# Kernel tuning notes

Measured on AMD Instinct MI355X. Metric: run time of the kernel, lower is better.

The kernel has to match this reference:

```python
import jax, jax.numpy as jnp
import numpy as np

B, S, H, E, K, DFF = 4, 2048, 1024, 8, 2, 4096


def setup_inputs() -> dict:
    key = jax.random.key(0)
    k0, k1, k2, k3 = jax.random.split(key, 4)
    sc = 0.02
    return {
        "x": jax.random.normal(k0, (B, S, H), jnp.float32),
        "gate_W": jax.random.normal(k1, (H, E), jnp.float32) * sc,
        "gate_b": jnp.zeros((E,), jnp.float32),
        "W1": jax.random.normal(k2, (H, DFF), jnp.float32) * sc,
        "b1": jnp.zeros((DFF,), jnp.float32),
        "W2": jax.random.normal(k3, (DFF, H), jnp.float32) * sc,
        "b2": jnp.zeros((H,), jnp.float32),
    }


def reference(x, gate_W, gate_b, W1, b1, W2, b2):
    b, s, h = x.shape
    x_flat = x.reshape(-1, h)                      # [T, H]
    gate_scores = x_flat @ gate_W + gate_b         # [T, E]
    top_k_scores, top_k_idx = jax.lax.top_k(gate_scores, K)   # [T, K]
    top_k_w = jax.nn.softmax(top_k_scores, axis=-1)           # [T, K]

    # All experts share the same weights (ModuleList reuses one module), so
    # sum_i w_i * expert_i(x) == expert(x) * sum_i w_i. top_k indices are
    # unique per token, so the per-token combine weight is sum of top-k weights.
    hdd = jax.nn.gelu(x_flat @ W1 + b1, approximate=False)    # [T, DFF]
    y = hdd @ W2 + b2                                         # [T, H]
    tok_w = top_k_w.sum(axis=-1)                              # [T] (== 1.0)
    output = (y * tok_w[:, None]).reshape(b, s, h)

    expert_load = gate_scores.mean(axis=0)                    # [E]
    aux_loss = (expert_load ** 2).sum()
    exp_counts = jnp.zeros((E,), jnp.int32).at[top_k_idx.ravel()].add(1)
    return output, aux_loss, exp_counts
```

## Files before the change

kernel.cpp:

```cpp
#include <hip/hip_runtime.h>
#include <hip/hip_bf16.h>
#include <math.h>

#define Tn   8192
#define Hn   1024
#define En   8
#define DFFn 4096

typedef __attribute__((ext_vector_type(8))) short bf16x8;
typedef __attribute__((ext_vector_type(8))) unsigned short u16x8;
typedef __attribute__((ext_vector_type(4))) float f32x4;

static __device__ inline unsigned short f2bf(float f) {
    __hip_bfloat16 h = __float2bfloat16(f);
    return __builtin_bit_cast(unsigned short, h);
}

__global__ __launch_bounds__(256) void prep(
    const float* __restrict__ W1, unsigned short* __restrict__ W1t,
    const float* __restrict__ W2, unsigned short* __restrict__ W2t,
    const float* __restrict__ x, const float* __restrict__ gW,
    const float* __restrict__ gb, unsigned short* __restrict__ xbf,
    float* __restrict__ tokw, float* __restrict__ pb_load,
    int* __restrict__ pb_cnt)
{
    __shared__ float smem[8 * 1024 + En];
    __shared__ int   s_cnt[En];
    const int tid = threadIdx.x;
    const int id  = blockIdx.x;

    if (id < 512) {
        const float* src; unsigned short* dst; int SR, SC, tb;
        if (id < 256) { src = W1; dst = W1t; SR = Hn;   SC = DFFn; tb = id; }
        else          { src = W2; dst = W2t; SR = DFFn; SC = Hn;   tb = id - 256; }
        const int tcs = SC >> 7;
        const int tr  = tb / tcs, tc = tb - tr * tcs;
        const int r0  = tr << 7, c0 = tc << 7;
        unsigned short* tile = (unsigned short*)smem;

        #pragma unroll
        for (int i = 0; i < 16; ++i) {
            int idx = tid + i * 256;
            int r = idx >> 5, c4 = (idx & 31) << 2;
            float4 v = *(const float4*)(src + (size_t)(r0 + r) * SC + c0 + c4);
            int cs = c4 ^ (((r >> 3) & 7) << 2);
            ushort4 pk;
            pk.x = f2bf(v.x); pk.y = f2bf(v.y);
            pk.z = f2bf(v.z); pk.w = f2bf(v.w);
            *(ushort4*)(tile + r * 128 + cs) = pk;
        }
        __syncthreads();
        #pragma unroll
        for (int i = 0; i < 8; ++i) {
            int idx = tid + i * 256;
            int n = idx >> 4, kg = idx & 15, k0 = kg << 3;
            int s = (kg & 7) << 2;
            u16x8 o;
            #pragma unroll
            for (int j = 0; j < 8; ++j)
                o[j] = tile[(k0 + j) * 128 + (n ^ s)];
            *(u16x8*)(dst + (size_t)(c0 + n) * SR + r0 + k0) = o;
        }
        return;
    }

    const int gid = id - 512;
    float* gwt    = smem;
    float* s_load = smem + 8 * 1024;
    if (tid < En) { s_load[tid] = 0.f; s_cnt[tid] = 0; }
    #pragma unroll
    for (int i = 0; i < 8; ++i) {
        int f4 = tid + i * 256;
        float4 v = ((const float4*)gW)[f4];
        int f = f4 << 2;
        gwt[((f + 0) & 7) * 1024 + ((f + 0) >> 3)] = v.x;
        gwt[((f + 1) & 7) * 1024 + ((f + 1) >> 3)] = v.y;
        gwt[((f + 2) & 7) * 1024 + ((f + 2) >> 3)] = v.z;
        gwt[((f + 3) & 7) * 1024 + ((f + 3) >> 3)] = v.w;
    }
    __syncthreads();

    const int lane = tid & 63;
    const int wv   = tid >> 6;

    for (int tok = gid * 4 + wv; tok < Tn; tok += 1024) {
        const float4* xr = (const float4*)(x + (size_t)tok * Hn);
        float acc[8] = {0.f,0.f,0.f,0.f,0.f,0.f,0.f,0.f};
        #pragma unroll
        for (int j = 0; j < Hn / 256; ++j) {
            int h4 = j * 64 + lane;
            float4 xv = xr[h4];
            ushort4 pk;
            pk.x = f2bf(xv.x); pk.y = f2bf(xv.y);
            pk.z = f2bf(xv.z); pk.w = f2bf(xv.w);
            ((ushort4*)xbf)[(size_t)tok * (Hn / 4) + h4] = pk;
            #pragma unroll
            for (int e = 0; e < 8; ++e) {
                const float4 w = *(const float4*)(gwt + e * 1024 + h4 * 4);
                acc[e] += xv.x * w.x + xv.y * w.y + xv.z * w.z + xv.w * w.w;
            }
        }
        #pragma unroll
        for (int e = 0; e < 8; ++e) {
            float v = acc[e];
            #pragma unroll
            for (int off = 32; off > 0; off >>= 1) v += __shfl_xor(v, off, 64);
            acc[e] = v + gb[e];
        }
        if (lane == 0) {
            #pragma unroll
            for (int e = 0; e < 8; ++e) atomicAdd(&s_load[e], acc[e]);
            int i1 = 0; float v1 = acc[0];
            #pragma unroll
            for (int e = 1; e < 8; ++e) if (acc[e] > v1) { v1 = acc[e]; i1 = e; }
            int i2 = -1; float v2 = -3.0e38f;
            #pragma unroll
            for (int e = 0; e < 8; ++e) if (e != i1 && acc[e] > v2) { v2 = acc[e]; i2 = e; }
            atomicAdd(&s_cnt[i1], 1);
            atomicAdd(&s_cnt[i2], 1);
            float e2 = __expf(v2 - v1);
            float t  = 1.0f + e2;
            tokw[tok] = 1.0f / t + e2 / t;
        }
    }
    __syncthreads();
    if (tid < En) {
        pb_load[gid * En + tid] = s_load[tid];
        pb_cnt [gid * En + tid] = s_cnt[tid];
    }
}

static __device__ inline bf16x8 ldsfrag(const char* base, int row, int chunk) {
    return *(const bf16x8*)(base + row * 128 + (((chunk) ^ (row & 7)) << 4));
}

template<int BN, int WM, int WN, int EPI>
__global__ __launch_bounds__(512, 2) void gemm8(
    const __hip_bfloat16* __restrict__ A,
    const __hip_bfloat16* __restrict__ Bt,
    const float* __restrict__ bias,
    const float* __restrict__ tokw,
    void* __restrict__ C, int N, int K, int nx,
    const float* __restrict__ pb_load, const int* __restrict__ pb_cnt,
    float* __restrict__ out_tail, int nblk)
{
    constexpr int BM = 256;
    constexpr int MR = (BM / WM) / 16;
    constexpr int NR = (BN / WN) / 16;
    constexpr int AU = BM / 64;
    constexpr int BU = BN / 64;
    constexpr int ABYTES = BM * 64 * 2;
    constexpr int BBYTES = BN * 64 * 2;
    constexpr int TILEB  = ABYTES + BBYTES;

    extern __shared__ char lds[];

    const int tid = threadIdx.x;
    const int id  = blockIdx.x;

    if (EPI == 0 && id >= nblk) {
        float* sl = (float*)lds;
        int*   sc = (int*)(lds + 64);
        if (tid < En) { sl[tid] = 0.f; sc[tid] = 0; }
        __syncthreads();
        const int e = tid & 7;
        float p = 0.f; int c = 0;
        for (int g = tid >> 3; g < 256; g += 64) {
            p += pb_load[g * En + e];
            c += pb_cnt [g * En + e];
        }
        atomicAdd(&sl[e], p);
        atomicAdd(&sc[e], c);
        __syncthreads();
        if (tid == 0) {
            float aux = 0.f;
            #pragma unroll
            for (int e2 = 0; e2 < En; ++e2) {
                float m = sl[e2] * (1.0f / (float)Tn);
                aux += m * m;
            }
            out_tail[0] = aux;
            #pragma unroll
            for (int e2 = 0; e2 < En; ++e2) out_tail[1 + e2] = (float)sc[e2];
        }
        return;
    }

    int wg = id;
    { int xcd = wg & 7, idx = wg >> 3; wg = xcd * (nblk >> 3) + idx; }
    const int by = wg / nx, bx = wg % nx;
    const int m0 = by * BM, n0 = bx * BN;

    const int lane = tid & 63;
    const int wid  = tid >> 6;
    const int wn   = wid % WN;
    const int wm   = wid / WN;
    const int wrow = wm * (BM / WM);
    const int wcol = wn * (BN / WN);
    const int fr   = lane & 15;
    const int fq   = lane >> 4;

    const int sr = tid >> 3;
    const int sc = (tid & 7) ^ (sr & 7);
    unsigned aOff[AU], bOff[BU];
    #pragma unroll
    for (int u = 0; u < AU; ++u)
        aOff[u] = (unsigned)((m0 + u * 64 + sr) * K + sc * 8);
    #pragma unroll
    for (int u = 0; u < BU; ++u)
        bOff[u] = (unsigned)((n0 + u * 64 + sr) * K + sc * 8);

#define STA(b, u, kt) __builtin_amdgcn_global_load_lds( \
    (const __attribute__((address_space(1))) void*)(A + aOff[u] + (unsigned)(kt) * 64u), \
    (__attribute__((address_space(3))) void*)(lds + (b) * TILEB + (u) * 8192 + tid * 16), 16, 0, 0)
#define STB(b, u, kt) __builtin_amdgcn_global_load_lds( \
    (const __attribute__((address_space(1))) void*)(Bt + bOff[u] + (unsigned)(kt) * 64u), \
    (__attribute__((address_space(3))) void*)(lds + (b) * TILEB + ABYTES + (u) * 8192 + tid * 16), 16, 0, 0)

    bf16x8 af[MR / 2][2];
    bf16x8 bfr[4][2];
    f32x4  acc[MR][NR];
    const f32x4 zero = {0.f, 0.f, 0.f, 0.f};
    #pragma unroll
    for (int i = 0; i < MR; ++i)
        #pragma unroll
        for (int j = 0; j < NR; ++j) acc[i][j] = zero;

#define RDA(b, half) do { _Pragma("unroll") \
    for (int m_ = 0; m_ < MR / 2; ++m_) { _Pragma("unroll") \
        for (int ks_ = 0; ks_ < 2; ++ks_) \
            af[m_][ks_] = ldsfrag(lds + (b) * TILEB, \
                wrow + ((half) * (MR / 2) + m_) * 16 + fr, ks_ * 4 + fq); } } while (0)

#define RDB(b, half) do { _Pragma("unroll") \
    for (int n_ = 0; n_ < 2; ++n_) { _Pragma("unroll") \
        for (int ks_ = 0; ks_ < 2; ++ks_) \
            bfr[(half) * 2 + n_][ks_] = ldsfrag(lds + (b) * TILEB + ABYTES, \
                wcol + ((half) * 2 + n_) * 16 + fr, ks_ * 4 + fq); } } while (0)

#define MFMAQ(hm, hn) do { \
    __builtin_amdgcn_s_setprio(1); \
    _Pragma("unroll") \
    for (int m_ = 0; m_ < MR / 2; ++m_) { _Pragma("unroll") \
        for (int n_ = 0; n_ < 2; ++n_) { _Pragma("unroll") \
            for (int ks_ = 0; ks_ < 2; ++ks_) \
                acc[(hm) * (MR / 2) + m_][(hn) * 2 + n_] = \
                    __builtin_amdgcn_mfma_f32_16x16x32_bf16( \
                        af[m_][ks_], bfr[(hn) * 2 + n_][ks_], \
                        acc[(hm) * (MR / 2) + m_][(hn) * 2 + n_], 0, 0, 0); } } \
    __builtin_amdgcn_s_setprio(0); } while (0)

#define MFMA1_N(hm, nn) do { _Pragma("unroll") \
    for (int m_ = 0; m_ < MR / 2; ++m_) { _Pragma("unroll") \
        for (int ks_ = 0; ks_ < 2; ++ks_) \
            acc[(hm) * (MR / 2) + m_][nn] = \
                __builtin_amdgcn_mfma_f32_16x16x32_bf16( \
                    bfr[nn][ks_], af[m_][ks_], \
                    acc[(hm) * (MR / 2) + m_][nn], 0, 0, 0); } } while (0)
#define MFMA1_M(hm, m_) do { _Pragma("unroll") \
    for (int n_ = 0; n_ < NR; ++n_) { _Pragma("unroll") \
        for (int ks_ = 0; ks_ < 2; ++ks_) \
            acc[(hm) * (MR / 2) + (m_)][n_] = \
                __builtin_amdgcn_mfma_f32_16x16x32_bf16( \
                    bfr[n_][ks_], af[m_][ks_], \
                    acc[(hm) * (MR / 2) + (m_)][n_], 0, 0, 0); } } while (0)

#define RD_A1(b, half, m_) do { _Pragma("unroll") \
    for (int ks_ = 0; ks_ < 2; ++ks_) \
        af[m_][ks_] = ldsfrag(lds + (b) * TILEB, \
            wrow + ((half) * (MR / 2) + (m_)) * 16 + fr, ks_ * 4 + fq); } while (0)
#define RD_B1(b, nn) do { _Pragma("unroll") \
    for (int ks_ = 0; ks_ < 2; ++ks_) \
        bfr[nn][ks_] = ldsfrag(lds + (b) * TILEB + ABYTES, \
            wcol + (nn) * 16 + fr, ks_ * 4 + fq); } while (0)

#define MIDSYNC do { \
    __builtin_amdgcn_sched_barrier(0); \
    __builtin_amdgcn_s_barrier(); \
    asm volatile("s_waitcnt lgkmcnt(0)" ::: "memory"); \
    __builtin_amdgcn_sched_barrier(0); } while (0)

#define SBARR do { \
    __builtin_amdgcn_sched_barrier(0); \
    __builtin_amdgcn_s_barrier(); \
    __builtin_amdgcn_sched_barrier(0); } while (0)

#define WAITL(n) do { \
    asm volatile("s_waitcnt lgkmcnt(" #n ")" ::: "memory"); \
    __builtin_amdgcn_sched_barrier(0); } while (0)

#define DRAIN6 do { asm volatile("s_waitcnt vmcnt(6)" ::: "memory"); \
    __builtin_amdgcn_sched_barrier(0); } while (0)
#define DRAIN2 do { asm volatile("s_waitcnt vmcnt(2)" ::: "memory"); \
    __builtin_amdgcn_sched_barrier(0); } while (0)
#define PRIO1 __builtin_amdgcn_s_setprio(1)
#define PRIO0 __builtin_amdgcn_s_setprio(0)

    const int KT = K >> 6;

    if constexpr (WM == 2) {
        STA(0,0,0); STA(0,1,0); STA(0,2,0); STA(0,3,0);
        STB(0,0,0); STB(0,1,0); STB(0,2,0); STB(0,3,0);
        STA(1,0,1); STA(1,2,1);
        STB(1,0,1); STB(1,1,1); STB(1,2,1); STB(1,3,1);
        DRAIN6;
        __builtin_amdgcn_s_barrier();
        __builtin_amdgcn_sched_barrier(0);

        for (int i = 0; i < (KT >> 1); ++i) {
            const int t1 = 2 * i + 1;
            const int c2 = (2 * i + 2 < KT) ? 2 * i + 2 : KT - 1;
            const int c3 = (2 * i + 3 < KT) ? 2 * i + 3 : KT - 1;

            RDA(0, 0); RDB(0, 0);
            STA(1,1,t1); STA(1,3,t1);
            MIDSYNC; MFMAQ(0, 0); SBARR;
            RDB(0, 1);
            STA(0,0,c2); STA(0,2,c2);
            MIDSYNC; MFMAQ(0, 1); SBARR;
            RDA(0, 1);
            STB(0,0,c2); STB(0,1,c2);
            MIDSYNC; MFMAQ(1, 0); SBARR;
            STB(0,2,c2); STB(0,3,c2);
            MIDSYNC; MFMAQ(1, 1); DRAIN6; SBARR;
            RDA(1, 0); RDB(1, 0);
            STA(0,1,c2); STA(0,3,c2);
            MIDSYNC; MFMAQ(0, 0); SBARR;
            RDB(1, 1);
            STA(1,0,c3); STA(1,2,c3);
            MIDSYNC; MFMAQ(0, 1); SBARR;
            RDA(1, 1);
            STB(1,0,c3); STB(1,1,c3);
            MIDSYNC; MFMAQ(1, 0); SBARR;
            STB(1,2,c3); STB(1,3,c3);
            MIDSYNC; MFMAQ(1, 1); DRAIN6; SBARR;
        }

        float bias4[NR];
        #pragma unroll
        for (int ni = 0; ni < NR; ++ni)
            bias4[ni] = bias[n0 + wcol + ni * 16 + fr];
        #pragma unroll
        for (int mi = 0; mi < MR; ++mi) {
            #pragma unroll
            for (int ni = 0; ni < NR; ++ni) {
                const int col = n0 + wcol + ni * 16 + fr;
                const int rb  = m0 + wrow + mi * 16 + fq * 4;
                #pragma unroll
                for (int i2 = 0; i2 < 4; ++i2) {
                    float u  = acc[mi][ni][i2] + bias4[ni];
                    float uu = u * u;
                    float z  = u * __fmaf_rn(uu, -0.07135607f, -1.59576912f);
                    float e  = __expf(z);
                    float g  = u * __builtin_amdgcn_rcpf(1.0f + e);
                    ((__hip_bfloat16*)C)[(size_t)(rb + i2) * N + col] =
                        __float2bfloat16(g);
                }
            }
        }
    } else {
        STA(0,0,0); STA(0,1,0); STA(0,2,0); STA(0,3,0);
        STB(0,0,0); STB(0,1,0);
        STB(1,0,1); STB(1,1,1);
        DRAIN2;
        __builtin_amdgcn_s_barrier();
        __builtin_amdgcn_sched_barrier(0);

        for (int i = 0; i < (KT >> 1); ++i) {
            const int t1 = 2 * i + 1;
            const int c2 = (2 * i + 2 < KT) ? 2 * i + 2 : KT - 1;
            const int c3 = (2 * i + 3 < KT) ? 2 * i + 3 : KT - 1;

            RD_A1(0,0,0); RD_A1(0,0,1);
            RD_B1(0,0); RD_B1(0,1); RD_B1(0,2); RD_B1(0,3);
            STA(1,0,t1); STA(1,1,t1); STA(1,2,t1); STA(1,3,t1);
            SBARR; PRIO1;
            WAITL(6); MFMA1_N(0,0);
            WAITL(4); MFMA1_N(0,1);
            WAITL(2); MFMA1_N(0,2);
            WAITL(0); MFMA1_N(0,3);
            PRIO0; SBARR;
            RD_A1(0,1,0); RD_A1(0,1,1);
            STB(0,0,c2); STB(0,1,c2);
            SBARR; PRIO1;
            WAITL(2); MFMA1_M(1,0);
            WAITL(0); MFMA1_M(1,1);
            PRIO0; DRAIN2; SBARR;
            RD_A1(1,0,0); RD_A1(1,0,1);
            RD_B1(1,0); RD_B1(1,1); RD_B1(1,2); RD_B1(1,3);
            STA(0,0,c2); STA(0,1,c2); STA(0,2,c2); STA(0,3,c2);
            SBARR; PRIO1;
            WAITL(6); MFMA1_N(0,0);
            WAITL(4); MFMA1_N(0,1);
            WAITL(2); MFMA1_N(0,2);
            WAITL(0); MFMA1_N(0,3);
            PRIO0; SBARR;
            RD_A1(1,1,0); RD_A1(1,1,1);
            STB(1,0,c3); STB(1,1,c3);
            SBARR; PRIO1;
            WAITL(2); MFMA1_M(1,0);
            WAITL(0); MFMA1_M(1,1);
            PRIO0; DRAIN2; SBARR;
        }

        const int mrow0 = m0 + wrow + fr;
        const int ncol0 = n0 + wcol + fq * 4;
        float4 b4[NR];
        #pragma unroll
        for (int ni = 0; ni < NR; ++ni)
            b4[ni] = *(const float4*)(bias + ncol0 + ni * 16);

        #pragma unroll
        for (int mi = 0; mi < MR; ++mi) {
            const int row = mrow0 + mi * 16;
            const float tw = tokw[row];
            #pragma unroll
            for (int ni = 0; ni < NR; ++ni) {
                f32x4 v = acc[mi][ni];
                float4 o;
                o.x = (v[0] + b4[ni].x) * tw;
                o.y = (v[1] + b4[ni].y) * tw;
                o.z = (v[2] + b4[ni].z) * tw;
                o.w = (v[3] + b4[ni].w) * tw;
                *(float4*)((float*)C + (size_t)row * N + ncol0 + ni * 16) = o;
            }
        }
    }

#undef STA
#undef STB
#undef RDA
#undef RDB
#undef RD_A1
#undef RD_B1
#undef MFMAQ
#undef MFMA1_N
#undef MFMA1_M
#undef MIDSYNC
#undef SBARR
#undef WAITL
#undef DRAIN6
#undef DRAIN2
#undef PRIO1
#undef PRIO0
}

extern "C" void kernel_launch(void* const* d_in, const int* in_sizes, int n_in,
                              void* d_out, int out_size, void* d_ws, size_t ws_size,
                              hipStream_t stream)
{
    const float* x  = (const float*)d_in[0];
    const float* gW = (const float*)d_in[1];
    const float* gb = (const float*)d_in[2];
    const float* W1 = (const float*)d_in[3];
    const float* b1 = (const float*)d_in[4];
    const float* W2 = (const float*)d_in[5];
    const float* b2 = (const float*)d_in[6];
    float* out = (float*)d_out;

    char* ws = (char*)d_ws;
    __hip_bfloat16* xbf = (__hip_bfloat16*)ws;  ws += (size_t)Tn * Hn * 2;
    __hip_bfloat16* W1t = (__hip_bfloat16*)ws;  ws += (size_t)Hn * DFFn * 2;
    __hip_bfloat16* W2t = (__hip_bfloat16*)ws;  ws += (size_t)Hn * DFFn * 2;
    __hip_bfloat16* hdd = (__hip_bfloat16*)ws;  ws += (size_t)Tn * DFFn * 2;
    float* tokw     = (float*)ws;               ws += (size_t)Tn * 4;
    float* pb_load  = (float*)ws;               ws += 256 * En * 4;
    int*   pb_cnt   = (int*)ws;                 ws += 256 * En * 4;

    static bool attr_done = false;
    if (!attr_done) {
        (void)hipFuncSetAttribute(
            reinterpret_cast<const void*>(&gemm8<256, 2, 4, 0>),
            hipFuncAttributeMaxDynamicSharedMemorySize, 131072);
        (void)hipFuncSetAttribute(
            reinterpret_cast<const void*>(&gemm8<128, 4, 2, 1>),
            hipFuncAttributeMaxDynamicSharedMemorySize, 98304);
        attr_done = true;
    }

    prep<<<768, 256, 0, stream>>>(W1, (unsigned short*)W1t,
                                  W2, (unsigned short*)W2t,
                                  x, gW, gb, (unsigned short*)xbf,
                                  tokw, pb_load, pb_cnt);

    gemm8<256, 2, 4, 0><<<513, 512, 131072, stream>>>(
        xbf, W1t, b1, nullptr, hdd, DFFn, Hn, 16,
        pb_load, pb_cnt, out + (size_t)Tn * Hn, 512);

    gemm8<128, 4, 2, 1><<<256, 512, 98304, stream>>>(
        hdd, W2t, b2, tokw, out, Hn, DFFn, 8,
        nullptr, nullptr, nullptr, 256);
}
```

Measured before the change: 262.9 us.

## Fuse prep and both GEMMs into one cooperative persistent kernel with grid syncs

```diff
diff --git a/kernel.cpp b/kernel.cpp
--- a/kernel.cpp
+++ b/kernel.cpp
@@ -1,6 +1,9 @@
 #include <hip/hip_runtime.h>
 #include <hip/hip_bf16.h>
+#include <hip/hip_cooperative_groups.h>
 #include <math.h>
+
+namespace cg = cooperative_groups;
 
 #define Tn   8192
 #define Hn   1024
@@ -16,161 +19,147 @@
     return __builtin_bit_cast(unsigned short, h);
 }
 
-__global__ __launch_bounds__(256) void prep(
-    const float* __restrict__ W1, unsigned short* __restrict__ W1t,
-    const float* __restrict__ W2, unsigned short* __restrict__ W2t,
-    const float* __restrict__ x, const float* __restrict__ gW,
-    const float* __restrict__ gb, unsigned short* __restrict__ xbf,
-    float* __restrict__ tokw, float* __restrict__ pb_load,
-    int* __restrict__ pb_cnt)
-{
-    __shared__ float smem[8 * 1024 + En];
-    __shared__ int   s_cnt[En];
-    const int tid = threadIdx.x;
-    const int id  = blockIdx.x;
-
-    if (id < 512) {
-        const float* src; unsigned short* dst; int SR, SC, tb;
-        if (id < 256) { src = W1; dst = W1t; SR = Hn;   SC = DFFn; tb = id; }
-        else          { src = W2; dst = W2t; SR = DFFn; SC = Hn;   tb = id - 256; }
-        const int tcs = SC >> 7;
-        const int tr  = tb / tcs, tc = tb - tr * tcs;
-        const int r0  = tr << 7, c0 = tc << 7;
-        unsigned short* tile = (unsigned short*)smem;
-
-        #pragma unroll
-        for (int i = 0; i < 16; ++i) {
-            int idx = tid + i * 256;
-            int r = idx >> 5, c4 = (idx & 31) << 2;
-            float4 v = *(const float4*)(src + (size_t)(r0 + r) * SC + c0 + c4);
-            int cs = c4 ^ (((r >> 3) & 7) << 2);
-            ushort4 pk;
-            pk.x = f2bf(v.x); pk.y = f2bf(v.y);
-            pk.z = f2bf(v.z); pk.w = f2bf(v.w);
-            *(ushort4*)(tile + r * 128 + cs) = pk;
-        }
-        __syncthreads();
-        #pragma unroll
-        for (int i = 0; i < 8; ++i) {
-            int idx = tid + i * 256;
-            int n = idx >> 4, kg = idx & 15, k0 = kg << 3;
-            int s = (kg & 7) << 2;
-            u16x8 o;
-            #pragma unroll
-            for (int j = 0; j < 8; ++j)
-                o[j] = tile[(k0 + j) * 128 + (n ^ s)];
-            *(u16x8*)(dst + (size_t)(c0 + n) * SR + r0 + k0) = o;
-        }
-        return;
-    }
-
-    const int gid = id - 512;
-    float* gwt    = smem;
-    float* s_load = smem + 8 * 1024;
-    if (tid < En) { s_load[tid] = 0.f; s_cnt[tid] = 0; }
-    #pragma unroll
-    for (int i = 0; i < 8; ++i) {
-        int f4 = tid + i * 256;
-        float4 v = ((const float4*)gW)[f4];
-        int f = f4 << 2;
-        gwt[((f + 0) & 7) * 1024 + ((f + 0) >> 3)] = v.x;
-        gwt[((f + 1) & 7) * 1024 + ((f + 1) >> 3)] = v.y;
-        gwt[((f + 2) & 7) * 1024 + ((f + 2) >> 3)] = v.z;
-        gwt[((f + 3) & 7) * 1024 + ((f + 3) >> 3)] = v.w;
-    }
-    __syncthreads();
-
-    const int lane = tid & 63;
-    const int wv   = tid >> 6;
-
-    for (int tok = gid * 4 + wv; tok < Tn; tok += 1024) {
-        const float4* xr = (const float4*)(x + (size_t)tok * Hn);
-        float acc[8] = {0.f,0.f,0.f,0.f,0.f,0.f,0.f,0.f};
-        #pragma unroll
-        for (int j = 0; j < Hn / 256; ++j) {
-            int h4 = j * 64 + lane;
-            float4 xv = xr[h4];
-            ushort4 pk;
-            pk.x = f2bf(xv.x); pk.y = f2bf(xv.y);
-            pk.z = f2bf(xv.z); pk.w = f2bf(xv.w);
-            ((ushort4*)xbf)[(size_t)tok * (Hn / 4) + h4] = pk;
-            #pragma unroll
-            for (int e = 0; e < 8; ++e) {
-                const float4 w = *(const float4*)(gwt + e * 1024 + h4 * 4);
-                acc[e] += xv.x * w.x + xv.y * w.y + xv.z * w.z + xv.w * w.w;
-            }
-        }
-        #pragma unroll
-        for (int e = 0; e < 8; ++e) {
-            float v = acc[e];
-            #pragma unroll
-            for (int off = 32; off > 0; off >>= 1) v += __shfl_xor(v, off, 64);
-            acc[e] = v + gb[e];
-        }
-        if (lane == 0) {
-            #pragma unroll
-            for (int e = 0; e < 8; ++e) atomicAdd(&s_load[e], acc[e]);
-            int i1 = 0; float v1 = acc[0];
-            #pragma unroll
-            for (int e = 1; e < 8; ++e) if (acc[e] > v1) { v1 = acc[e]; i1 = e; }
-            int i2 = -1; float v2 = -3.0e38f;
-            #pragma unroll
-            for (int e = 0; e < 8; ++e) if (e != i1 && acc[e] > v2) { v2 = acc[e]; i2 = e; }
-            atomicAdd(&s_cnt[i1], 1);
-            atomicAdd(&s_cnt[i2], 1);
-            float e2 = __expf(v2 - v1);
-            float t  = 1.0f + e2;
-            tokw[tok] = 1.0f / t + e2 / t;
-        }
-    }
-    __syncthreads();
-    if (tid < En) {
-        pb_load[gid * En + tid] = s_load[tid];
-        pb_cnt [gid * En + tid] = s_cnt[tid];
-    }
-}
-
 static __device__ inline bf16x8 ldsfrag(const char* base, int row, int chunk) {
     return *(const bf16x8*)(base + row * 128 + (((chunk) ^ (row & 7)) << 4));
 }
 
-template<int BN, int WM, int WN, int EPI>
-__global__ __launch_bounds__(512, 2) void gemm8(
-    const __hip_bfloat16* __restrict__ A,
-    const __hip_bfloat16* __restrict__ Bt,
-    const float* __restrict__ bias,
-    const float* __restrict__ tokw,
-    void* __restrict__ C, int N, int K, int nx,
-    const float* __restrict__ pb_load, const int* __restrict__ pb_cnt,
-    float* __restrict__ out_tail, int nblk)
+__global__ __launch_bounds__(512, 2) void moe_fused(
+    const float* __restrict__ x,  const float* __restrict__ gW,
+    const float* __restrict__ gb, const float* __restrict__ W1,
+    const float* __restrict__ b1, const float* __restrict__ W2,
+    const float* __restrict__ b2,
+    unsigned short* __restrict__ W1t, unsigned short* __restrict__ W2t,
+    unsigned short* __restrict__ xbf, unsigned short* __restrict__ hdd,
+    float* __restrict__ tokw, float* __restrict__ pb_load,
+    int* __restrict__ pb_cnt, float* __restrict__ out,
+    float* __restrict__ out_tail)
 {
-    constexpr int BM = 256;
-    constexpr int MR = (BM / WM) / 16;
-    constexpr int NR = (BN / WN) / 16;
-    constexpr int AU = BM / 64;
-    constexpr int BU = BN / 64;
-    constexpr int ABYTES = BM * 64 * 2;
-    constexpr int BBYTES = BN * 64 * 2;
-    constexpr int TILEB  = ABYTES + BBYTES;
-
     extern __shared__ char lds[];
-
     const int tid = threadIdx.x;
-    const int id  = blockIdx.x;
-
-    if (EPI == 0 && id >= nblk) {
+    const int bid = blockIdx.x;
+    const int lane = tid & 63;
+    const int wid  = tid >> 6;
+    const int fr   = lane & 15;
+    const int fq   = lane >> 4;
+    const int sr   = tid >> 3;
+    const int scq  = (tid & 7) ^ (sr & 7);
+
+    {
+        unsigned short* tile = (unsigned short*)lds;
+        #pragma unroll
+        for (int pass = 0; pass < 2; ++pass) {
+            const float* src = pass ? W2 : W1;
+            unsigned short* dst = pass ? W2t : W1t;
+            const int SR = pass ? DFFn : Hn, SC = pass ? Hn : DFFn;
+            const int tcs = SC >> 7;
+            const int tr = bid / tcs, tc = bid - tr * tcs;
+            const int r0 = tr << 7, c0 = tc << 7;
+            #pragma unroll
+            for (int i = 0; i < 8; ++i) {
+                int idx = tid + i * 512;
+                int r = idx >> 5, c4 = (idx & 31) << 2;
+                float4 v = *(const float4*)(src + (size_t)(r0 + r) * SC + c0 + c4);
+                int cs = c4 ^ (((r >> 3) & 7) << 2);
+                ushort4 pk;
+                pk.x = f2bf(v.x); pk.y = f2bf(v.y);
+                pk.z = f2bf(v.z); pk.w = f2bf(v.w);
+                *(ushort4*)(tile + r * 128 + cs) = pk;
+            }
+            __syncthreads();
+            #pragma unroll
+            for (int i = 0; i < 4; ++i) {
+                int idx = tid + i * 512;
+                int n = idx >> 4, kg = idx & 15, k0 = kg << 3;
+                int s = (kg & 7) << 2;
+                u16x8 o;
+                #pragma unroll
+                for (int j = 0; j < 8; ++j)
+                    o[j] = tile[(k0 + j) * 128 + (n ^ s)];
+                *(u16x8*)(dst + (size_t)(c0 + n) * SR + r0 + k0) = o;
+            }
+            __syncthreads();
+        }
+
+        float* gwt    = (float*)lds;
+        float* s_load = (float*)(lds + 32768);
+        int*   s_cnt  = (int*)(lds + 32768 + 64);
+        if (tid < En) { s_load[tid] = 0.f; s_cnt[tid] = 0; }
+        #pragma unroll
+        for (int i = 0; i < 4; ++i) {
+            int f4 = tid + i * 512;
+            float4 v = ((const float4*)gW)[f4];
+            int f = f4 << 2;
+            gwt[((f + 0) & 7) * 1024 + ((f + 0) >> 3)] = v.x;
+            gwt[((f + 1) & 7) * 1024 + ((f + 1) >> 3)] = v.y;
+            gwt[((f + 2) & 7) * 1024 + ((f + 2) >> 3)] = v.z;
+            gwt[((f + 3) & 7) * 1024 + ((f + 3) >> 3)] = v.w;
+        }
+        __syncthreads();
+        #pragma unroll
+        for (int t = 0; t < 4; ++t) {
+            const int tok = bid * 32 + wid + t * 8;
+            const float4* xr = (const float4*)(x + (size_t)tok * Hn);
+            float acc[8] = {0.f,0.f,0.f,0.f,0.f,0.f,0.f,0.f};
+            #pragma unroll
+            for (int j = 0; j < Hn / 256; ++j) {
+                int h4 = j * 64 + lane;
+                float4 xv = xr[h4];
+                ushort4 pk;
+                pk.x = f2bf(xv.x); pk.y = f2bf(xv.y);
+                pk.z = f2bf(xv.z); pk.w = f2bf(xv.w);
+                ((ushort4*)xbf)[(size_t)tok * (Hn / 4) + h4] = pk;
+                #pragma unroll
+                for (int e = 0; e < 8; ++e) {
+                    const float4 w = *(const float4*)(gwt + e * 1024 + h4 * 4);
+                    acc[e] += xv.x * w.x + xv.y * w.y + xv.z * w.z + xv.w * w.w;
+                }
+            }
+            #pragma unroll
+            for (int e = 0; e < 8; ++e) {
+                float v = acc[e];
+                #pragma unroll
+                for (int off = 32; off > 0; off >>= 1) v += __shfl_xor(v, off, 64);
+                acc[e] = v + gb[e];
+            }
+            if (lane == 0) {
+                #pragma unroll
+                for (int e = 0; e < 8; ++e) atomicAdd(&s_load[e], acc[e]);
+                int i1 = 0; float v1 = acc[0];
+                #pragma unroll
+                for (int e = 1; e < 8; ++e) if (acc[e] > v1) { v1 = acc[e]; i1 = e; }
+                int i2 = -1; float v2 = -3.0e38f;
+                #pragma unroll
+                for (int e = 0; e < 8; ++e) if (e != i1 && acc[e] > v2) { v2 = acc[e]; i2 = e; }
+                atomicAdd(&s_cnt[i1], 1);
+                atomicAdd(&s_cnt[i2], 1);
+                float e2 = __expf(v2 - v1);
+                float tt = 1.0f + e2;
+                tokw[tok] = 1.0f / tt + e2 / tt;
+            }
+        }
+        __syncthreads();
+        if (tid < En) {
+            pb_load[bid * En + tid] = s_load[tid];
+            pb_cnt [bid * En + tid] = s_cnt[tid];
+        }
+    }
+
+    __threadfence();
+    cg::this_grid().sync();
+
+    if (bid == 0) {
         float* sl = (float*)lds;
-        int*   sc = (int*)(lds + 64);
-        if (tid < En) { sl[tid] = 0.f; sc[tid] = 0; }
+        int*   scp = (int*)(lds + 64);
+        if (tid < En) { sl[tid] = 0.f; scp[tid] = 0; }
         __syncthreads();
         const int e = tid & 7;
         float p = 0.f; int c = 0;
-        for (int g = tid >> 3; g < 256; g += 64) {
-            p += pb_load[g * En + e];
-            c += pb_cnt [g * En + e];
+        for (int g2 = tid >> 3; g2 < 256; g2 += 64) {
+            p += pb_load[g2 * En + e];
+            c += pb_cnt [g2 * En + e];
         }
         atomicAdd(&sl[e], p);
-        atomicAdd(&sc[e], c);
+        atomicAdd(&scp[e], c);
         __syncthreads();
         if (tid == 0) {
             float aux = 0.f;
@@ -181,266 +170,305 @@
             }
             out_tail[0] = aux;
             #pragma unroll
-            for (int e2 = 0; e2 < En; ++e2) out_tail[1 + e2] = (float)sc[e2];
-        }
-        return;
+            for (int e2 = 0; e2 < En; ++e2) out_tail[1 + e2] = (float)scp[e2];
+        }
+        __syncthreads();
     }
 
-    int wg = id;
-    { int xcd = wg & 7, idx = wg >> 3; wg = xcd * (nblk >> 3) + idx; }
-    const int by = wg / nx, bx = wg % nx;
-    const int m0 = by * BM, n0 = bx * BN;
-
-    const int lane = tid & 63;
-    const int wid  = tid >> 6;
-    const int wn   = wid % WN;
-    const int wm   = wid / WN;
-    const int wrow = wm * (BM / WM);
-    const int wcol = wn * (BN / WN);
-    const int fr   = lane & 15;
-    const int fq   = lane >> 4;
-
-    const int sr = tid >> 3;
-    const int sc = (tid & 7) ^ (sr & 7);
-    unsigned aOff[AU], bOff[BU];
-    #pragma unroll
-    for (int u = 0; u < AU; ++u)
-        aOff[u] = (unsigned)((m0 + u * 64 + sr) * K + sc * 8);
-    #pragma unroll
-    for (int u = 0; u < BU; ++u)
-        bOff[u] = (unsigned)((n0 + u * 64 + sr) * K + sc * 8);
-
-#define STA(b, u, kt) __builtin_amdgcn_global_load_lds( \
-    (const __attribute__((address_space(1))) void*)(A + aOff[u] + (unsigned)(kt) * 64u), \
-    (__attribute__((address_space(3))) void*)(lds + (b) * TILEB + (u) * 8192 + tid * 16), 16, 0, 0)
-#define STB(b, u, kt) __builtin_amdgcn_global_load_lds( \
-    (const __attribute__((address_space(1))) void*)(Bt + bOff[u] + (unsigned)(kt) * 64u), \
-    (__attribute__((address_space(3))) void*)(lds + (b) * TILEB + ABYTES + (u) * 8192 + tid * 16), 16, 0, 0)
-
-    bf16x8 af[MR / 2][2];
-    bf16x8 bfr[4][2];
-    f32x4  acc[MR][NR];
-    const f32x4 zero = {0.f, 0.f, 0.f, 0.f};
-    #pragma unroll
-    for (int i = 0; i < MR; ++i)
-        #pragma unroll
-        for (int j = 0; j < NR; ++j) acc[i][j] = zero;
-
-#define RDA(b, half) do { _Pragma("unroll") \
-    for (int m_ = 0; m_ < MR / 2; ++m_) { _Pragma("unroll") \
-        for (int ks_ = 0; ks_ < 2; ++ks_) \
-            af[m_][ks_] = ldsfrag(lds + (b) * TILEB, \
-                wrow + ((half) * (MR / 2) + m_) * 16 + fr, ks_ * 4 + fq); } } while (0)
-
-#define RDB(b, half) do { _Pragma("unroll") \
-    for (int n_ = 0; n_ < 2; ++n_) { _Pragma("unroll") \
-        for (int ks_ = 0; ks_ < 2; ++ks_) \
-            bfr[(half) * 2 + n_][ks_] = ldsfrag(lds + (b) * TILEB + ABYTES, \
-                wcol + ((half) * 2 + n_) * 16 + fr, ks_ * 4 + fq); } } while (0)
-
-#define MFMAQ(hm, hn) do { \
-    __builtin_amdgcn_s_setprio(1); \
-    _Pragma("unroll") \
-    for (int m_ = 0; m_ < MR / 2; ++m_) { _Pragma("unroll") \
-        for (int n_ = 0; n_ < 2; ++n_) { _Pragma("unroll") \
-            for (int ks_ = 0; ks_ < 2; ++ks_) \
-                acc[(hm) * (MR / 2) + m_][(hn) * 2 + n_] = \
-                    __builtin_amdgcn_mfma_f32_16x16x32_bf16( \
-                        af[m_][ks_], bfr[(hn) * 2 + n_][ks_], \
-                        acc[(hm) * (MR / 2) + m_][(hn) * 2 + n_], 0, 0, 0); } } \
-    __builtin_amdgcn_s_setprio(0); } while (0)
-
-#define MFMA1_N(hm, nn) do { _Pragma("unroll") \
-    for (int m_ = 0; m_ < MR / 2; ++m_) { _Pragma("unroll") \
-        for (int ks_ = 0; ks_ < 2; ++ks_) \
-            acc[(hm) * (MR / 2) + m_][nn] = \
-                __builtin_amdgcn_mfma_f32_16x16x32_bf16( \
-                    bfr[nn][ks_], af[m_][ks_], \
-                    acc[(hm) * (MR / 2) + m_][nn], 0, 0, 0); } } while (0)
-#define MFMA1_M(hm, m_) do { _Pragma("unroll") \
-    for (int n_ = 0; n_ < NR; ++n_) { _Pragma("unroll") \
-        for (int ks_ = 0; ks_ < 2; ++ks_) \
-            acc[(hm) * (MR / 2) + (m_)][n_] = \
-                __builtin_amdgcn_mfma_f32_16x16x32_bf16( \
-                    bfr[n_][ks_], af[m_][ks_], \
-                    acc[(hm) * (MR / 2) + (m_)][n_], 0, 0, 0); } } while (0)
-
-#define RD_A1(b, half, m_) do { _Pragma("unroll") \
-    for (int ks_ = 0; ks_ < 2; ++ks_) \
-        af[m_][ks_] = ldsfrag(lds + (b) * TILEB, \
-            wrow + ((half) * (MR / 2) + (m_)) * 16 + fr, ks_ * 4 + fq); } while (0)
-#define RD_B1(b, nn) do { _Pragma("unroll") \
-    for (int ks_ = 0; ks_ < 2; ++ks_) \
-        bfr[nn][ks_] = ldsfrag(lds + (b) * TILEB + ABYTES, \
-            wcol + (nn) * 16 + fr, ks_ * 4 + fq); } while (0)
-
+#define SBARR do { \
+    __builtin_amdgcn_sched_barrier(0); \
+    __builtin_amdgcn_s_barrier(); \
+    __builtin_amdgcn_sched_barrier(0); } while (0)
 #define MIDSYNC do { \
     __builtin_amdgcn_sched_barrier(0); \
     __builtin_amdgcn_s_barrier(); \
     asm volatile("s_waitcnt lgkmcnt(0)" ::: "memory"); \
     __builtin_amdgcn_sched_barrier(0); } while (0)
-
-#define SBARR do { \
-    __builtin_amdgcn_sched_barrier(0); \
-    __builtin_amdgcn_s_barrier(); \
-    __builtin_amdgcn_sched_barrier(0); } while (0)
-
 #define WAITL(n) do { \
     asm volatile("s_waitcnt lgkmcnt(" #n ")" ::: "memory"); \
     __builtin_amdgcn_sched_barrier(0); } while (0)
-
-#define DRAIN6 do { asm volatile("s_waitcnt vmcnt(6)" ::: "memory"); \
-    __builtin_amdgcn_sched_barrier(0); } while (0)
-#define DRAIN2 do { asm volatile("s_waitcnt vmcnt(2)" ::: "memory"); \
+#define VMC(n) do { asm volatile("s_waitcnt vmcnt(" #n ")" ::: "memory"); \
     __builtin_amdgcn_sched_barrier(0); } while (0)
 #define PRIO1 __builtin_amdgcn_s_setprio(1)
 #define PRIO0 __builtin_amdgcn_s_setprio(0)
 
-    const int KT = K >> 6;
-
-    if constexpr (WM == 2) {
-        STA(0,0,0); STA(0,1,0); STA(0,2,0); STA(0,3,0);
-        STB(0,0,0); STB(0,1,0); STB(0,2,0); STB(0,3,0);
-        STA(1,0,1); STA(1,2,1);
-        STB(1,0,1); STB(1,1,1); STB(1,2,1); STB(1,3,1);
-        DRAIN6;
+    {
+        constexpr int ABY = 256 * 64 * 2;
+        constexpr int TLB = ABY + ABY;
+        const int wn = wid & 3, wm = wid >> 2;
+        const int wrow = wm * 128, wcol = wn * 64;
+
+        bf16x8 af[4][2], bfr[4][2];
+        f32x4  acc[8][4];
+        const f32x4 zero = {0.f, 0.f, 0.f, 0.f};
+
+#define STA0(b, u, kt) __builtin_amdgcn_global_load_lds( \
+    (const __attribute__((address_space(1))) void*)(xbf + aOff[u] + (unsigned)(kt) * 64u), \
+    (__attribute__((address_space(3))) void*)(lds + (b) * TLB + (u) * 8192 + tid * 16), 16, 0, 0)
+#define STB0(b, u, kt) __builtin_amdgcn_global_load_lds( \
+    (const __attribute__((address_space(1))) void*)(W1t + bOff[u] + (unsigned)(kt) * 64u), \
+    (__attribute__((address_space(3))) void*)(lds + (b) * TLB + ABY + (u) * 8192 + tid * 16), 16, 0, 0)
+#define RDA0(b, half) do { _Pragma("unroll") \
+    for (int m_ = 0; m_ < 4; ++m_) { _Pragma("unroll") \
+        for (int ks_ = 0; ks_ < 2; ++ks_) \
+            af[m_][ks_] = ldsfrag(lds + (b) * TLB, \
+                wrow + ((half) * 4 + m_) * 16 + fr, ks_ * 4 + fq); } } while (0)
+#define RDB0(b, half) do { _Pragma("unroll") \
+    for (int n_ = 0; n_ < 2; ++n_) { _Pragma("unroll") \
+        for (int ks_ = 0; ks_ < 2; ++ks_) \
+            bfr[(half) * 2 + n_][ks_] = ldsfrag(lds + (b) * TLB + ABY, \
+                wcol + ((half) * 2 + n_) * 16 + fr, ks_ * 4 + fq); } } while (0)
+#define MFMAQ0(hm, hn) do { \
+    PRIO1; \
+    _Pragma("unroll") \
+    for (int m_ = 0; m_ < 4; ++m_) { _Pragma("unroll") \
+        for (int n_ = 0; n_ < 2; ++n_) { _Pragma("unroll") \
+            for (int ks_ = 0; ks_ < 2; ++ks_) \
+                acc[(hm) * 4 + m_][(hn) * 2 + n_] = \
+                    __builtin_amdgcn_mfma_f32_16x16x32_bf16( \
+                        af[m_][ks_], bfr[(hn) * 2 + n_][ks_], \
+                        acc[(hm) * 4 + m_][(hn) * 2 + n_], 0, 0, 0); } } \
+    PRIO0; } while (0)
+
+        for (int tt = 0; tt < 2; ++tt) {
+            const int g   = bid + tt * 256;
+            const int xcd = g & 7;
+            const int wg  = xcd * 64 + (g >> 3);
+            const int by  = wg >> 4, bx = wg & 15;
+            const int m0  = by * 256, n0 = bx * 256;
+
+            unsigned aOff[4], bOff[4];
+            #pragma unroll
+            for (int u = 0; u < 4; ++u) {
+                aOff[u] = (unsigned)((m0 + u * 64 + sr) * Hn + scq * 8);
+                bOff[u] = (unsigned)((n0 + u * 64 + sr) * Hn + scq * 8);
+            }
+            #pragma unroll
+            for (int i = 0; i < 8; ++i)
+                #pragma unroll
+                for (int j = 0; j < 4; ++j) acc[i][j] = zero;
+
+            STA0(0,0,0); STA0(0,1,0); STA0(0,2,0); STA0(0,3,0);
+            STB0(0,0,0); STB0(0,1,0); STB0(0,2,0); STB0(0,3,0);
+            STA0(1,0,1); STA0(1,2,1);
+            STB0(1,0,1); STB0(1,1,1); STB0(1,2,1); STB0(1,3,1);
+            VMC(6);
+            __builtin_amdgcn_s_barrier();
+            __builtin_amdgcn_sched_barrier(0);
+
+            const int KT = Hn >> 6;
+            for (int i = 0; i < (KT >> 1); ++i) {
+                const int t1 = 2 * i + 1;
+                const int c2 = (2 * i + 2 < KT) ? 2 * i + 2 : KT - 1;
+                const int c3 = (2 * i + 3 < KT) ? 2 * i + 3 : KT - 1;
+
+                RDA0(0, 0); RDB0(0, 0);
+                STA0(1,1,t1); STA0(1,3,t1);
+                MIDSYNC; MFMAQ0(0, 0); SBARR;
+
+                RDB0(0, 1);
+                STA0(0,0,c2); STA0(0,2,c2);
+                MIDSYNC; MFMAQ0(0, 1); SBARR;
+
+                RDA0(0, 1);
+                STB0(0,0,c2); STB0(0,1,c2);
+                MIDSYNC; MFMAQ0(1, 0); SBARR;
+
+                STB0(0,2,c2); STB0(0,3,c2);
+                MIDSYNC; MFMAQ0(1, 1); VMC(6); SBARR;
+
+                RDA0(1, 0); RDB0(1, 0);
+                STA0(0,1,c2); STA0(0,3,c2);
+                MIDSYNC; MFMAQ0(0, 0); SBARR;
+
+                RDB0(1, 1);
+                STA0(1,0,c3); STA0(1,2,c3);
+                MIDSYNC; MFMAQ0(0, 1); SBARR;
+
+                RDA0(1, 1);
+                STB0(1,0,c3); STB0(1,1,c3);
+                MIDSYNC; MFMAQ0(1, 0); SBARR;
+
+                STB0(1,2,c3); STB0(1,3,c3);
+                MIDSYNC; MFMAQ0(1, 1); VMC(6); SBARR;
+            }
+
+            float bias4[4];
+            #pragma unroll
+            for (int ni = 0; ni < 4; ++ni)
+                bias4[ni] = b1[n0 + wcol + ni * 16 + fr];
+            #pragma unroll
+            for (int mi = 0; mi < 8; ++mi) {
+                #pragma unroll
+                for (int ni = 0; ni < 4; ++ni) {
+                    const int col = n0 + wcol + ni * 16 + fr;
+                    const int rb  = m0 + wrow + mi * 16 + fq * 4;
+                    #pragma unroll
+                    for (int i2 = 0; i2 < 4; ++i2) {
+                        float u  = acc[mi][ni][i2] + bias4[ni];
+                        float uu = u * u;
+                        float z  = u * __fmaf_rn(uu, -0.07135607f, -1.59576912f);
+                        float e  = __expf(z);
+                        float gg = u * __builtin_amdgcn_rcpf(1.0f + e);
+                        hdd[(size_t)(rb + i2) * DFFn + col] = f2bf(gg);
+                    }
+                }
+            }
+            if (tt == 0) {
+                asm volatile("s_waitcnt vmcnt(0)" ::: "memory");
+                __builtin_amdgcn_sched_barrier(0);
+                SBARR;
+            }
+        }
+#undef STA0
+#undef STB0
+#undef RDA0
+#undef RDB0
+#undef MFMAQ0
+    }
+
+    __threadfence();
+    cg::this_grid().sync();
+
+    {
+        constexpr int ABY = 256 * 64 * 2;
+        constexpr int BBY = 128 * 64 * 2;
+        constexpr int TLB = ABY + BBY;
+        const int wn = wid & 1, wm = wid >> 1;
+        const int wrow = wm * 64, wcol = wn * 64;
+
+        bf16x8 af[2][2], bfr[4][2];
+        f32x4  acc[4][4];
+        const f32x4 zero = {0.f, 0.f, 0.f, 0.f};
+        #pragma unroll
+        for (int i = 0; i < 4; ++i)
+            #pragma unroll
+            for (int j = 0; j < 4; ++j) acc[i][j] = zero;
+
+        const int g   = bid;
+        const int xcd = g & 7;
+        const int wg  = xcd * 32 + (g >> 3);
+        const int by  = wg >> 3, bx = wg & 7;
+        const int m0  = by * 256, n0 = bx * 128;
+
+        unsigned aOff[4], bOff[2];
+        #pragma unroll
+        for (int u = 0; u < 4; ++u)
+            aOff[u] = (unsigned)((m0 + u * 64 + sr) * DFFn + scq * 8);
+        #pragma unroll
+        for (int u = 0; u < 2; ++u)
+            bOff[u] = (unsigned)((n0 + u * 64 + sr) * DFFn + scq * 8);
+
+#define STA1(b, u, kt) __builtin_amdgcn_global_load_lds( \
+    (const __attribute__((address_space(1))) void*)(hdd + aOff[u] + (unsigned)(kt) * 64u), \
+    (__attribute__((address_space(3))) void*)(lds + (b) * TLB + (u) * 8192 + tid * 16), 16, 0, 0)
+#define STB1(b, u, kt) __builtin_amdgcn_global_load_lds( \
+    (const __attribute__((address_space(1))) void*)(W2t + bOff[u] + (unsigned)(kt) * 64u), \
+    (__attribute__((address_space(3))) void*)(lds + (b) * TLB + ABY + (u) * 8192 + tid * 16), 16, 0, 0)
+#define RD_A1(b, half, m_) do { _Pragma("unroll") \
+    for (int ks_ = 0; ks_ < 2; ++ks_) \
+        af[m_][ks_] = ldsfrag(lds + (b) * TLB, \
+            wrow + ((half) * 2 + (m_)) * 16 + fr, ks_ * 4 + fq); } while (0)
+#define RD_B1(b, nn) do { _Pragma("unroll") \
+    for (int ks_ = 0; ks_ < 2; ++ks_) \
+        bfr[nn][ks_] = ldsfrag(lds + (b) * TLB + ABY, \
+            wcol + (nn) * 16 + fr, ks_ * 4 + fq); } while (0)
+#define MFMA1_N(hm, nn) do { _Pragma("unroll") \
+    for (int m_ = 0; m_ < 2; ++m_) { _Pragma("unroll") \
+        for (int ks_ = 0; ks_ < 2; ++ks_) \
+            acc[(hm) * 2 + m_][nn] = \
+                __builtin_amdgcn_mfma_f32_16x16x32_bf16( \
+                    bfr[nn][ks_], af[m_][ks_], \
+                    acc[(hm) * 2 + m_][nn], 0, 0, 0); } } while (0)
+#define MFMA1_M(hm, m_) do { _Pragma("unroll") \
+    for (int n_ = 0; n_ < 4; ++n_) { _Pragma("unroll") \
+        for (int ks_ = 0; ks_ < 2; ++ks_) \
+            acc[(hm) * 2 + (m_)][n_] = \
+                __builtin_amdgcn_mfma_f32_16x16x32_bf16( \
+                    bfr[n_][ks_], af[m_][ks_], \
+                    acc[(hm) * 2 + (m_)][n_], 0, 0, 0); } } while (0)
+
+        STA1(0,0,0); STA1(0,1,0); STA1(0,2,0); STA1(0,3,0);
+        STB1(0,0,0); STB1(0,1,0);
+        STB1(1,0,1); STB1(1,1,1);
+        VMC(2);
         __builtin_amdgcn_s_barrier();
         __builtin_amdgcn_sched_barrier(0);
 
+        const int KT = DFFn >> 6;
         for (int i = 0; i < (KT >> 1); ++i) {
             const int t1 = 2 * i + 1;
             const int c2 = (2 * i + 2 < KT) ? 2 * i + 2 : KT - 1;
             const int c3 = (2 * i + 3 < KT) ? 2 * i + 3 : KT - 1;
 
-            RDA(0, 0); RDB(0, 0);
-            STA(1,1,t1); STA(1,3,t1);
-            MIDSYNC; MFMAQ(0, 0); SBARR;
-            RDB(0, 1);
-            STA(0,0,c2); STA(0,2,c2);
-            MIDSYNC; MFMAQ(0, 1); SBARR;
-            RDA(0, 1);
-            STB(0,0,c2); STB(0,1,c2);
-            MIDSYNC; MFMAQ(1, 0); SBARR;
-            STB(0,2,c2); STB(0,3,c2);
-            MIDSYNC; MFMAQ(1, 1); DRAIN6; SBARR;
-            RDA(1, 0); RDB(1, 0);
-            STA(0,1,c2); STA(0,3,c2);
-            MIDSYNC; MFMAQ(0, 0); SBARR;
-            RDB(1, 1);
-            STA(1,0,c3); STA(1,2,c3);
-            MIDSYNC; MFMAQ(0, 1); SBARR;
-            RDA(1, 1);
-            STB(1,0,c3); STB(1,1,c3);
-            MIDSYNC; MFMAQ(1, 0); SBARR;
-            STB(1,2,c3); STB(1,3,c3);
-            MIDSYNC; MFMAQ(1, 1); DRAIN6; SBARR;
-        }
-
-        float bias4[NR];
-        #pragma unroll
-        for (int ni = 0; ni < NR; ++ni)
-            bias4[ni] = bias[n0 + wcol + ni * 16 + fr];
-        #pragma unroll
-        for (int mi = 0; mi < MR; ++mi) {
-            #pragma unroll
-            for (int ni = 0; ni < NR; ++ni) {
-                const int col = n0 + wcol + ni * 16 + fr;
-                const int rb  = m0 + wrow + mi * 16 + fq * 4;
-                #pragma unroll
-                for (int i2 = 0; i2 < 4; ++i2) {
-                    float u  = acc[mi][ni][i2] + bias4[ni];
-                    float uu = u * u;
-                    float z  = u * __fmaf_rn(uu, -0.07135607f, -1.59576912f);
-                    float e  = __expf(z);
-                    float g  = u * __builtin_amdgcn_rcpf(1.0f + e);
-                    ((__hip_bfloat16*)C)[(size_t)(rb + i2) * N + col] =
-                        __float2bfloat16(g);
-                }
-            }
-        }
-    } else {
-        STA(0,0,0); STA(0,1,0); STA(0,2,0); STA(0,3,0);
-        STB(0,0,0); STB(0,1,0);
-        STB(1,0,1); STB(1,1,1);
-        DRAIN2;
-        __builtin_amdgcn_s_barrier();
-        __builtin_amdgcn_sched_barrier(0);
-
-        for (int i = 0; i < (KT >> 1); ++i) {
-            const int t1 = 2 * i + 1;
-            const int c2 = (2 * i + 2 < KT) ? 2 * i + 2 : KT - 1;
-            const int c3 = (2 * i + 3 < KT) ? 2 * i + 3 : KT - 1;
-
             RD_A1(0,0,0); RD_A1(0,0,1);
             RD_B1(0,0); RD_B1(0,1); RD_B1(0,2); RD_B1(0,3);
-            STA(1,0,t1); STA(1,1,t1); STA(1,2,t1); STA(1,3,t1);
+            STA1(1,0,t1); STA1(1,1,t1); STA1(1,2,t1); STA1(1,3,t1);
             SBARR; PRIO1;
             WAITL(6); MFMA1_N(0,0);
             WAITL(4); MFMA1_N(0,1);
             WAITL(2); MFMA1_N(0,2);
             WAITL(0); MFMA1_N(0,3);
             PRIO0; SBARR;
+
             RD_A1(0,1,0); RD_A1(0,1,1);
-            STB(0,0,c2); STB(0,1,c2);
+            STB1(0,0,c2); STB1(0,1,c2);
             SBARR; PRIO1;
             WAITL(2); MFMA1_M(1,0);
             WAITL(0); MFMA1_M(1,1);
-            PRIO0; DRAIN2; SBARR;
+            PRIO0; VMC(2); SBARR;
+
             RD_A1(1,0,0); RD_A1(1,0,1);
             RD_B1(1,0); RD_B1(1,1); RD_B1(1,2); RD_B1(1,3);
-            STA(0,0,c2); STA(0,1,c2); STA(0,2,c2); STA(0,3,c2);
+            STA1(0,0,c2); STA1(0,1,c2); STA1(0,2,c2); STA1(0,3,c2);
             SBARR; PRIO1;
             WAITL(6); MFMA1_N(0,0);
             WAITL(4); MFMA1_N(0,1);
             WAITL(2); MFMA1_N(0,2);
             WAITL(0); MFMA1_N(0,3);
             PRIO0; SBARR;
+
             RD_A1(1,1,0); RD_A1(1,1,1);
-            STB(1,0,c3); STB(1,1,c3);
+            STB1(1,0,c3); STB1(1,1,c3);
             SBARR; PRIO1;
             WAITL(2); MFMA1_M(1,0);
             WAITL(0); MFMA1_M(1,1);
-            PRIO0; DRAIN2; SBARR;
+            PRIO0; VMC(2); SBARR;
         }
 
         const int mrow0 = m0 + wrow + fr;
         const int ncol0 = n0 + wcol + fq * 4;
-        float4 b4[NR];
-        #pragma unroll
-        for (int ni = 0; ni < NR; ++ni)
-            b4[ni] = *(const float4*)(bias + ncol0 + ni * 16);
-
-        #pragma unroll
-        for (int mi = 0; mi < MR; ++mi) {
+        float4 b4[4];
+        #pragma unroll
+        for (int ni = 0; ni < 4; ++ni)
+            b4[ni] = *(const float4*)(b2 + ncol0 + ni * 16);
+
+        #pragma unroll
+        for (int mi = 0; mi < 4; ++mi) {
             const int row = mrow0 + mi * 16;
             const float tw = tokw[row];
             #pragma unroll
-            for (int ni = 0; ni < NR; ++ni) {
+            for (int ni = 0; ni < 4; ++ni) {
                 f32x4 v = acc[mi][ni];
                 float4 o;
                 o.x = (v[0] + b4[ni].x) * tw;
                 o.y = (v[1] + b4[ni].y) * tw;
                 o.z = (v[2] + b4[ni].z) * tw;
                 o.w = (v[3] + b4[ni].w) * tw;
-                *(float4*)((float*)C + (size_t)row * N + ncol0 + ni * 16) = o;
-            }
-        }
-    }
-
-#undef STA
-#undef STB
-#undef RDA
-#undef RDB
+                *(float4*)(out + (size_t)row * Hn + ncol0 + ni * 16) = o;
+            }
+        }
+#undef STA1
+#undef STB1
 #undef RD_A1
 #undef RD_B1
-#undef MFMAQ
 #undef MFMA1_N
 #undef MFMA1_M
+    }
+#undef SBARR
 #undef MIDSYNC
-#undef SBARR
 #undef WAITL
-#undef DRAIN6
-#undef DRAIN2
+#undef VMC
 #undef PRIO1
 #undef PRIO0
 }
@@ -459,35 +487,30 @@
     float* out = (float*)d_out;
 
     char* ws = (char*)d_ws;
-    __hip_bfloat16* xbf = (__hip_bfloat16*)ws;  ws += (size_t)Tn * Hn * 2;
-    __hip_bfloat16* W1t = (__hip_bfloat16*)ws;  ws += (size_t)Hn * DFFn * 2;
-    __hip_bfloat16* W2t = (__hip_bfloat16*)ws;  ws += (size_t)Hn * DFFn * 2;
-    __hip_bfloat16* hdd = (__hip_bfloat16*)ws;  ws += (size_t)Tn * DFFn * 2;
+    unsigned short* xbf = (unsigned short*)ws;  ws += (size_t)Tn * Hn * 2;
+    unsigned short* W1t = (unsigned short*)ws;  ws += (size_t)Hn * DFFn * 2;
+    unsigned short* W2t = (unsigned short*)ws;  ws += (size_t)Hn * DFFn * 2;
+    unsigned short* hdd = (unsigned short*)ws;  ws += (size_t)Tn * DFFn * 2;
     float* tokw     = (float*)ws;               ws += (size_t)Tn * 4;
     float* pb_load  = (float*)ws;               ws += 256 * En * 4;
     int*   pb_cnt   = (int*)ws;                 ws += 256 * En * 4;
+    float* out_tail = out + (size_t)Tn * Hn;
 
     static bool attr_done = false;
     if (!attr_done) {
         (void)hipFuncSetAttribute(
-            reinterpret_cast<const void*>(&gemm8<256, 2, 4, 0>),
+            reinterpret_cast<const void*>(&moe_fused),
             hipFuncAttributeMaxDynamicSharedMemorySize, 131072);
-        (void)hipFuncSetAttribute(
-            reinterpret_cast<const void*>(&gemm8<128, 4, 2, 1>),
-            hipFuncAttributeMaxDynamicSharedMemorySize, 98304);
         attr_done = true;
     }
 
-    prep<<<768, 256, 0, stream>>>(W1, (unsigned short*)W1t,
-                                  W2, (unsigned short*)W2t,
-                                  x, gW, gb, (unsigned short*)xbf,
-                                  tokw, pb_load, pb_cnt);
-
-    gemm8<256, 2, 4, 0><<<513, 512, 131072, stream>>>(
-        xbf, W1t, b1, nullptr, hdd, DFFn, Hn, 16,
-        pb_load, pb_cnt, out + (size_t)Tn * Hn, 512);
-
-    gemm8<128, 4, 2, 1><<<256, 512, 98304, stream>>>(
-        hdd, W2t, b2, tokw, out, Hn, DFFn, 8,
-        nullptr, nullptr, nullptr, 256);
+    void* kargs[] = {
+        (void*)&x, (void*)&gW, (void*)&gb, (void*)&W1, (void*)&b1,
+        (void*)&W2, (void*)&b2, (void*)&W1t, (void*)&W2t, (void*)&xbf,
+        (void*)&hdd, (void*)&tokw, (void*)&pb_load, (void*)&pb_cnt,
+        (void*)&out, (void*)&out_tail
+    };
+    (void)hipLaunchCooperativeKernel(
+        reinterpret_cast<const void*>(&moe_fused),
+        dim3(256), dim3(512), kargs, 131072, stream);
 }
```

New measurement: 462.2 us. 75.8% more time.
